# Kernel tuning notes

Measured on AMD Instinct MI355X. Metric: run time of the kernel, lower is better.

The kernel has to match this reference:

```python
import jax, jax.numpy as jnp
import numpy as np

MODEL_DIM = 2048
HEAD_DIM = 64
STATE_DIM = 128
EXPAND = 2
CHUNK = 64
INNER = EXPAND * MODEL_DIM          # 4096
NHEADS = INNER // HEAD_DIM          # 64
IN_PROJ = INNER + 2 * STATE_DIM + NHEADS  # 4416
B_SZ = 2
SEQ = 4096


def segsum(x):
    """Stable segment sum: x (..., T) -> (..., T, T) with -inf above diagonal."""
    T = x.shape[-1]
    mask_strict = jnp.tril(jnp.ones((T, T), dtype=bool), -1)
    # element [d, e] = x[d] on strictly-lower triangle, 0 elsewhere
    xt = jnp.where(mask_strict, x[..., :, None], 0.0)
    seg = jnp.cumsum(xt, axis=-2)
    mask = jnp.tril(jnp.ones((T, T), dtype=bool), 0)
    return jnp.where(mask, seg, -jnp.inf)


def ssd(x, A, B, C, chunk):
    """Mamba-2 SSD. x:(b,L,h,p), A:(b,L,h), B/C:(b,L,n) shared over heads."""
    b, L, h, p = x.shape
    n = B.shape[-1]
    c = L // chunk
    x = x.reshape(b, c, chunk, h, p)
    A = A.reshape(b, c, chunk, h).transpose(0, 3, 1, 2)  # (b,h,c,l)
    B = B.reshape(b, c, chunk, n)
    C = C.reshape(b, c, chunk, n)

    A_cs = jnp.cumsum(A, axis=-1)                        # (b,h,c,l)
    Lm = jnp.exp(segsum(A))                              # (b,h,c,l,l)
    # 1. diagonal (intra-chunk) output
    Y_diag = jnp.einsum('bcln,bcsn,bhcls,bcshp->bclhp', C, B, Lm, x)
    # 2. per-chunk states
    decay_states = jnp.exp(A_cs[..., -1:] - A_cs)        # (b,h,c,l)
    states = jnp.einsum('bcln,bhcl,bclhp->bchpn', B, decay_states, x)
    states = jnp.concatenate([jnp.zeros_like(states[:, :1]), states], axis=1)
    # 3. inter-chunk recurrence
    A_chunk = jnp.pad(A_cs[..., -1], ((0, 0), (0, 0), (1, 0)))   # (b,h,c+1)
    decay_chunk = jnp.exp(segsum(A_chunk))               # (b,h,c+1,c+1)
    new_states = jnp.einsum('bhzc,bchpn->bzhpn', decay_chunk, states)
    states_prev, final_state = new_states[:, :-1], new_states[:, -1]
    # 4. state -> output
    Y_off = jnp.einsum('bcln,bchpn,bhcl->bclhp', C, states_prev, jnp.exp(A_cs))
    Y = (Y_diag + Y_off).reshape(b, L, h, p)
    return Y, final_state


def setup_inputs() -> dict:
    key = jax.random.key(0)
    ks = jax.random.split(key, 6)
    u = jax.random.normal(ks[0], (B_SZ, SEQ, MODEL_DIM), jnp.float32)
    W_in = jax.random.normal(ks[1], (IN_PROJ, MODEL_DIM), jnp.float32) * 0.02
    b_in = jnp.zeros((IN_PROJ,), jnp.float32)
    W_out = jax.random.normal(ks[2], (MODEL_DIM, INNER), jnp.float32) * 0.02
    b_out = jnp.zeros((MODEL_DIM,), jnp.float32)
    # A_log = log(uniform(1, 16)) per Mamba-2 init
    A_log = jnp.log(jax.random.uniform(ks[3], (NHEADS,), jnp.float32, 1.0, 16.0))
    # dt_bias = inv-softplus of dt ~ loguniform(1e-3, 1e-1)
    dt = jnp.exp(jax.random.uniform(ks[4], (NHEADS,), jnp.float32)
                 * (np.log(0.1) - np.log(0.001)) + np.log(0.001))
    dt = jnp.clip(dt, 1e-4, None)
    dt_bias = dt + jnp.log(-jnp.expm1(-dt))
    return {'u': u, 'W_in': W_in, 'b_in': b_in, 'W_out': W_out,
            'b_out': b_out, 'A_log': A_log, 'dt_bias': dt_bias}


def reference(u, W_in, b_in, W_out, b_out, A_log, dt_bias):
    xBCdt = u @ W_in.T + b_in                       # (b, L, IN_PROJ)
    x, Bm, Cm, dt = jnp.split(
        xBCdt, [INNER, INNER + STATE_DIM, INNER + 2 * STATE_DIM], axis=-1)
    A = -jnp.exp(A_log)                             # (h,)
    dt = jax.nn.softplus(dt + dt_bias)              # (b, L, h)
    x = x.reshape(B_SZ, SEQ, NHEADS, HEAD_DIM)
    y, final_state = ssd(x * dt[..., None], A * dt, Bm, Cm, CHUNK)
    y = y.reshape(B_SZ, SEQ, INNER)
    y = y @ W_out.T + b_out
    return y, final_state
```

## Files before the change

kernel.cpp:

```cpp
#include <hip/hip_runtime.h>
#include <hip/hip_bf16.h>

typedef __hip_bfloat16 bf16;
typedef __attribute__((ext_vector_type(8))) short short8;
typedef __attribute__((ext_vector_type(4))) float f32x4;

#define MODEL_DIM 2048
#define INNER     4096
#define NHEADS    64
#define HEAD_DIM  64
#define STATE_DIM 128
#define IN_PROJ   4416
#define BSZ       2
#define SEQ       4096
#define CHUNKL    64
#define NTOK      (BSZ*SEQ)
#define NCHUNK    (SEQ/CHUNKL)

#define WAITV0() asm volatile("s_waitcnt vmcnt(0)" ::: "memory")
#define BAR()    __builtin_amdgcn_s_barrier()
#define SCHEDB() __builtin_amdgcn_sched_barrier(0)
#define WAITLG(N) do { asm volatile("s_waitcnt lgkmcnt(" #N ")" ::: "memory"); SCHEDB(); } while (0)

#define SWZ(x) ((x) ^ ((((x) >> 7) & 7) << 4))

static __device__ __forceinline__ void gload_lds16(const bf16* g, bf16* l) {
  __builtin_amdgcn_global_load_lds((const __attribute__((address_space(1))) void*)g,
                                   (__attribute__((address_space(3))) void*)l, 16, 0, 0);
}

static __device__ __forceinline__ unsigned lds_u32(const void* p) {
  return (unsigned)(unsigned long long)(const __attribute__((address_space(3))) char*)p;
}

static __device__ __forceinline__ short8 ds_read128(unsigned addr) {
  short8 r;
  asm volatile("ds_read_b128 %0, %1" : "=v"(r) : "v"(addr));
  return r;
}

static __device__ __forceinline__ void stage_unit(const bf16* __restrict__ P, int K,
                                                  int blockRow, int kt,
                                                  char* region, int unit, int t) {
  int o = unit * 8192 + (t << 4);
  int lb = SWZ(o);
  int row = lb >> 7, colb = lb & 127;
  gload_lds16(P + (size_t)(blockRow + row) * K + kt + (colb >> 1), (bf16*)(region + o));
}

#define MFMA_BLK(MLO, MHI, NLO, NHI)                                                    \
  __builtin_amdgcn_s_setprio(1);                                                       \
  _Pragma("unroll") for (int mf = (MLO); mf < (MHI); ++mf)                             \
    _Pragma("unroll") for (int nf = (NLO); nf < (NHI); ++nf)                           \
      _Pragma("unroll") for (int ks = 0; ks < 2; ++ks)                                 \
        acc[mf][nf] = __builtin_amdgcn_mfma_f32_16x16x32_bf16(a[mf][ks], b[nf][ks],    \
                                                              acc[mf][nf], 0, 0, 0);  \
  __builtin_amdgcn_s_setprio(0);

template<int BN>
static __device__ __forceinline__ void gemm_core1(
    const bf16* __restrict__ Ag, const bf16* __restrict__ Bg,
    int K, int NT, int bm, int bn, char* lds, f32x4 (&acc)[8][BN / 64]) {
  constexpr int NR = BN / 64;
  constexpr int BB = 32768 + NR * 8192;
  const int t = threadIdx.x;
  const int lane = t & 63;
  const int wid = t >> 6, wm = wid >> 2, wn = wid & 3;
  const unsigned x16 = (unsigned)(lane & 7) << 4;
  const unsigned kb0 = (unsigned)(lane >> 4) << 4;
  const unsigned ldsB = lds_u32(lds);
  const unsigned aRow0 = (unsigned)(wm * 128 + (lane & 15)) * 128;
  const unsigned bRow0 = (unsigned)(wn * (BN / 4) + (lane & 15)) * 128;

#pragma unroll
  for (int u = 0; u < 4; ++u) stage_unit(Ag, K, bm, 0, lds, u, t);
#pragma unroll
  for (int u = 0; u < NR; ++u) stage_unit(Bg, K, bn, 0, lds + 32768, u, t);
  WAITV0();
  BAR();

  int cur = 0;
  for (int tt = 0; tt < NT; ++tt) {
    char* oth = lds + (cur ^ 1) * BB;
    const unsigned aB = ldsB + (unsigned)(cur * BB);
    const unsigned bB = aB + 32768;
    const bool st = (tt + 1 < NT);

    if (st) {
      const int kt1 = (tt + 1) * 64;
#pragma unroll
      for (int u = 0; u < 4; ++u) stage_unit(Ag, K, bm, kt1, oth, u, t);
#pragma unroll
      for (int u = 0; u < NR; ++u) stage_unit(Bg, K, bn, kt1, oth + 32768, u, t);
    }

    short8 a[8][2], b[NR][2];
#pragma unroll
    for (int mf = 0; mf < 4; ++mf)
#pragma unroll
      for (int ks = 0; ks < 2; ++ks)
        a[mf][ks] = ds_read128(aB + aRow0 + mf * 2048 + (((unsigned)(ks * 64) + kb0) ^ x16));
#pragma unroll
    for (int nf = 0; nf < 2; ++nf)
#pragma unroll
      for (int ks = 0; ks < 2; ++ks)
        b[nf][ks] = ds_read128(bB + bRow0 + nf * 2048 + (((unsigned)(ks * 64) + kb0) ^ x16));
#pragma unroll
    for (int mf = 4; mf < 8; ++mf)
#pragma unroll
      for (int ks = 0; ks < 2; ++ks)
        a[mf][ks] = ds_read128(aB + aRow0 + mf * 2048 + (((unsigned)(ks * 64) + kb0) ^ x16));
#pragma unroll
    for (int nf = 2; nf < NR; ++nf)
#pragma unroll
      for (int ks = 0; ks < 2; ++ks)
        b[nf][ks] = ds_read128(bB + bRow0 + nf * 2048 + (((unsigned)(ks * 64) + kb0) ^ x16));

    if constexpr (NR == 4) WAITLG(12); else WAITLG(10);
    MFMA_BLK(0, 4, 0, 2);
    if constexpr (NR == 4) WAITLG(4);  else WAITLG(2);
    MFMA_BLK(4, 8, 0, 2);
    WAITLG(0);
    MFMA_BLK(0, 8, 2, NR);

    if (st) WAITV0();
    BAR();
    cur ^= 1;
  }
}

__global__ __launch_bounds__(512, 2)
void gemm_in256(const bf16* __restrict__ A, const bf16* __restrict__ Bw,
                const float* __restrict__ bias, bf16* __restrict__ x_bf,
                bf16* __restrict__ B_bf, bf16* __restrict__ C_bf, float* __restrict__ dtraw) {
  __shared__ char lds[2 * (32768 + 3 * 8192)];
  int nwg = gridDim.x, bid = blockIdx.x;
  int cpx = nwg >> 3;
  int sb = (bid & 7) * cpx + (bid >> 3);
  int bx = sb % (IN_PROJ / 192), by = sb / (IN_PROJ / 192);
  int bm = by * 256, bn = bx * 192;
  f32x4 acc[8][3] = {};
  gemm_core1<192>(A, Bw, MODEL_DIM, MODEL_DIM / 64, bm, bn, lds, acc);
  const int lane = threadIdx.x & 63, wid = threadIdx.x >> 6;
  const int wm = wid >> 2, wn = wid & 3;
#pragma unroll
  for (int mf = 0; mf < 8; ++mf)
#pragma unroll
    for (int nf = 0; nf < 3; ++nf)
#pragma unroll
      for (int r = 0; r < 4; ++r) {
        int row = bm + wm * 128 + mf * 16 + (lane >> 4) * 4 + r;
        int col = bn + wn * 48 + nf * 16 + (lane & 15);
        float v = acc[mf][nf][r] + bias[col];
        if (col < 4096)       x_bf[(size_t)row * 4096 + col]         = __float2bfloat16(v);
        else if (col < 4224)  B_bf[(size_t)row * 128 + (col - 4096)] = __float2bfloat16(v);
        else if (col < 4352)  C_bf[(size_t)row * 128 + (col - 4224)] = __float2bfloat16(v);
        else                  dtraw[(size_t)row * 64 + (col - 4352)] = v;
      }
}

__global__ __launch_bounds__(512, 2)
void gemm_out256(const bf16* __restrict__ A, const bf16* __restrict__ Bw,
                 const float* __restrict__ bias, float* __restrict__ C) {
  __shared__ char lds[2 * (32768 + 4 * 8192)];
  int nwg = gridDim.x, bid = blockIdx.x;
  int cpx = nwg >> 3;
  int sb = (bid & 7) * cpx + (bid >> 3);
  int bx = sb % (MODEL_DIM / 256), by = sb / (MODEL_DIM / 256);
  int bm = by * 256, bn = bx * 256;
  f32x4 acc[8][4] = {};
  gemm_core1<256>(A, Bw, INNER, INNER / 64, bm, bn, lds, acc);
  const int lane = threadIdx.x & 63, wid = threadIdx.x >> 6;
  const int wm = wid >> 2, wn = wid & 3;
#pragma unroll
  for (int mf = 0; mf < 8; ++mf)
#pragma unroll
    for (int nf = 0; nf < 4; ++nf)
#pragma unroll
      for (int r = 0; r < 4; ++r) {
        int row = bm + wm * 128 + mf * 16 + (lane >> 4) * 4 + r;
        int col = bn + wn * 64 + nf * 16 + (lane & 15);
        C[(size_t)row * MODEL_DIM + col] = acc[mf][nf][r] + bias[col];
      }
}

__global__ __launch_bounds__(256) void conv_f32_to_bf16(const float* __restrict__ src,
                                                        bf16* __restrict__ dst, int n4) {
  int i = blockIdx.x * 256 + threadIdx.x;
  if (i >= n4) return;
  float4 v = *(const float4*)(src + (size_t)i * 4);
  bf16* d = dst + (size_t)i * 4;
  d[0] = __float2bfloat16(v.x); d[1] = __float2bfloat16(v.y);
  d[2] = __float2bfloat16(v.z); d[3] = __float2bfloat16(v.w);
}

__global__ __launch_bounds__(256)
void prep_small(const float* __restrict__ dtraw, const float* __restrict__ A_log,
                const float* __restrict__ dt_bias, float* __restrict__ dts,
                float* __restrict__ a_dt) {
  int i = blockIdx.x * 256 + threadIdx.x;
  int h = i & 63;
  float z = dtraw[i] + dt_bias[h];
  float dt = (z > 20.f) ? z : log1pf(expf(z));
  dts[i] = dt;
  a_dt[i] = -expf(A_log[h]) * dt;
}

__global__ __launch_bounds__(256)
void g_pre_kernel(const bf16* __restrict__ B_bf, const bf16* __restrict__ C_bf,
                  float* __restrict__ G_g) {
  __shared__ bf16 Cs[64 * 128];
  __shared__ bf16 Bs[64 * 128];
  int blk = blockIdx.x;
  int t = threadIdx.x, lane = t & 63, wid = t >> 6;
  int tokBase = (blk >> 6) * SEQ + (blk & 63) * 64;

#pragma unroll
  for (int i = 0; i < 4; ++i) {
    int chunk = t + i * 256;
    int l = chunk >> 4, n0 = (chunk & 15) * 8;
    *(short8*)(Cs + l * 128 + n0) = *(const short8*)(C_bf + (size_t)(tokBase + l) * 128 + n0);
    *(short8*)(Bs + l * 128 + n0) = *(const short8*)(B_bf + (size_t)(tokBase + l) * 128 + n0);
  }
  __syncthreads();

  int lBase = (wid >> 1) * 32, sBase = (wid & 1) * 32;
  f32x4 g[2][2] = {};
#pragma unroll
  for (int ks = 0; ks < 4; ++ks) {
    short8 a[2], bb[2];
#pragma unroll
    for (int mi = 0; mi < 2; ++mi)
      a[mi] = *(const short8*)(Cs + (lBase + mi * 16 + (lane & 15)) * 128 + ks * 32 + (lane >> 4) * 8);
#pragma unroll
    for (int ni = 0; ni < 2; ++ni)
      bb[ni] = *(const short8*)(Bs + (sBase + ni * 16 + (lane & 15)) * 128 + ks * 32 + (lane >> 4) * 8);
#pragma unroll
    for (int mi = 0; mi < 2; ++mi)
#pragma unroll
      for (int ni = 0; ni < 2; ++ni)
        g[mi][ni] = __builtin_amdgcn_mfma_f32_16x16x32_bf16(a[mi], bb[ni], g[mi][ni], 0, 0, 0);
  }
  float* Gd = G_g + (size_t)blk * 4096;
#pragma unroll
  for (int mi = 0; mi < 2; ++mi)
#pragma unroll
    for (int ni = 0; ni < 2; ++ni)
#pragma unroll
      for (int r = 0; r < 4; ++r) {
        int row = lBase + mi * 16 + (lane >> 4) * 4 + r;
        int col = sBase + ni * 16 + (lane & 15);
        Gd[row * 64 + col] = g[mi][ni][r];
      }
}

#define LP 72
__global__ __launch_bounds__(256)
void ssd_fused_kernel(const bf16* __restrict__ x_bf, const bf16* __restrict__ B_bf,
                      const float* __restrict__ dts_g, const float* __restrict__ a_dt,
                      float* __restrict__ acs_g, bf16* __restrict__ states_g,
                      float* __restrict__ out_fs) {
  __shared__ bf16 xT[2][32 * LP];
  __shared__ bf16 BT[2][128 * LP];
  __shared__ float sc_s[64];
  __shared__ float dfac_s[1];
  int blk = blockIdx.x;
  int pg = blk & 1, h = (blk >> 1) & 63, b = blk >> 7;
  int t = threadIdx.x, lane = t & 63, w = t >> 6;
  int lx = t >> 2, sx = t & 3;
  int lB = t >> 2, sB = t & 3;

  f32x4 S4[4] = {};
  short8 rx, rB[4]; float ra = 0.f, rdt = 0.f;
  {
    int tb = b * SEQ;
    rx = *(const short8*)(x_bf + (size_t)(tb + lx) * 4096 + h * 64 + pg * 32 + sx * 8);
#pragma unroll
    for (int k = 0; k < 4; ++k)
      rB[k] = *(const short8*)(B_bf + (size_t)(tb + lB) * 128 + sB * 32 + k * 8);
    if (t < 64) { ra = a_dt[(size_t)(tb + t) * 64 + h]; rdt = dts_g[(size_t)(tb + t) * 64 + h]; }
  }

  for (int c = 0; c < 64; ++c) {
    int cn = (c < 63) ? c + 1 : 63;
    int tbn = b * SEQ + cn * 64;
    short8 rx2 = *(const short8*)(x_bf + (size_t)(tbn + lx) * 4096 + h * 64 + pg * 32 + sx * 8);
    short8 rB2[4];
#pragma unroll
    for (int k = 0; k < 4; ++k)
      rB2[k] = *(const short8*)(B_bf + (size_t)(tbn + lB) * 128 + sB * 32 + k * 8);
    float ra2 = 0.f, rdt2 = 0.f;
    if (t < 64) { ra2 = a_dt[(size_t)(tbn + t) * 64 + h]; rdt2 = dts_g[(size_t)(tbn + t) * 64 + h]; }

    if (t < 64) {
      float v = ra;
#pragma unroll
      for (int d = 1; d < 64; d <<= 1) { float o = __shfl_up(v, d); if (t >= d) v += o; }
      float a63 = __shfl(v, 63);
      if (pg == 0) acs_g[(((size_t)(b * 64 + c)) * 64 + h) * 64 + t] = v;
      sc_s[t] = rdt * expf(a63 - v);
      if (t == 0) dfac_s[0] = expf(a63);
    }
    __syncthreads();

    int bufc = c & 1;
    float dfac = dfac_s[0];
    {
      float s_l = sc_s[lx];
      const bf16* pv = (const bf16*)&rx;
#pragma unroll
      for (int j = 0; j < 8; ++j)
        xT[bufc][(sx * 8 + j) * LP + lx] = __float2bfloat16(__bfloat162float(pv[j]) * s_l);
#pragma unroll
      for (int k = 0; k < 4; ++k) {
        const bf16* pb = (const bf16*)&rB[k];
        int n0 = sB * 32 + k * 8;
#pragma unroll
        for (int j = 0; j < 8; ++j) BT[bufc][(n0 + j) * LP + lB] = pb[j];
      }
    }
    __syncthreads();

    int ps = (w >> 1) * 16, nb = (w & 1) * 64;
    f32x4 acc[4] = {};
    short8 af[2];
#pragma unroll
    for (int ks = 0; ks < 2; ++ks)
      af[ks] = *(const short8*)(&xT[bufc][(ps + (lane & 15)) * LP + ks * 32 + (lane >> 4) * 8]);
#pragma unroll
    for (int nf = 0; nf < 4; ++nf)
#pragma unroll
      for (int ks = 0; ks < 2; ++ks) {
        short8 bf_ = *(const short8*)(&BT[bufc][(nb + nf * 16 + (lane & 15)) * LP + ks * 32 + (lane >> 4) * 8]);
        acc[nf] = __builtin_amdgcn_mfma_f32_16x16x32_bf16(af[ks], bf_, acc[nf], 0, 0, 0);
      }
    size_t sbase = ((size_t)((b * 64 + c) * 64 + h)) * 8192;
#pragma unroll
    for (int nf = 0; nf < 4; ++nf)
#pragma unroll
      for (int r = 0; r < 4; ++r) {
        int p = pg * 32 + ps + (lane >> 4) * 4 + r;
        int n = nb + nf * 16 + (lane & 15);
        states_g[sbase + (size_t)p * 128 + n] = __float2bfloat16(S4[nf][r]);
        S4[nf][r] = dfac * S4[nf][r] + acc[nf][r];
      }

    rx = rx2; ra = ra2; rdt = rdt2;
#pragma unroll
    for (int k = 0; k < 4; ++k) rB[k] = rB2[k];
  }

  size_t ob = ((size_t)(b * 64 + h)) * 8192;
  int ps = (w >> 1) * 16, nb = (w & 1) * 64;
#pragma unroll
  for (int nf = 0; nf < 4; ++nf)
#pragma unroll
    for (int r = 0; r < 4; ++r) {
      int p = pg * 32 + ps + (lane >> 4) * 4 + r;
      int n = nb + nf * 16 + (lane & 15);
      out_fs[ob + (size_t)p * 128 + n] = S4[nf][r];
    }
}

__global__ __launch_bounds__(256)
void ssd_out_kernel(bf16* __restrict__ x_bf, const bf16* __restrict__ C_bf,
                    const float* __restrict__ dts, const float* __restrict__ acs_g,
                    const bf16* __restrict__ states_g, const float* __restrict__ G_g) {
  __shared__ bf16 Cs[64 * 128];
  __shared__ bf16 Ms[64 * 64];
  __shared__ bf16 xT[64 * 64];
  __shared__ bf16 Sp[64 * 128];
  __shared__ float acs_s[64];
  int blk = blockIdx.x;
  int h = blk & 63, c = (blk >> 6) & 63, b = blk >> 12;
  int t = threadIdx.x, lane = t & 63, wid = t >> 6;
  int tokBase = b * SEQ + c * 64;
  size_t sbase = ((size_t)((b * 64 + c) * 64 + h)) * 8192;

  int lBase = (wid >> 1) * 32, sBase = (wid & 1) * 32;
  const float* Gd = G_g + ((size_t)(b * 64 + c)) * 4096;
  float gv[2][2][4];
#pragma unroll
  for (int mi = 0; mi < 2; ++mi)
#pragma unroll
    for (int ni = 0; ni < 2; ++ni)
#pragma unroll
      for (int r = 0; r < 4; ++r)
        gv[mi][ni][r] = Gd[(lBase + mi * 16 + (lane >> 4) * 4 + r) * 64 +
                           sBase + ni * 16 + (lane & 15)];

  if (t < 64) acs_s[t] = acs_g[(((size_t)(b * 64 + c)) * 64 + h) * 64 + t];
#pragma unroll
  for (int i = 0; i < 4; ++i) {
    int chunk = t + i * 256;
    int l = chunk >> 4, n0 = (chunk & 15) * 8;
    *(short8*)(Cs + l * 128 + n0) = *(const short8*)(C_bf + (size_t)(tokBase + l) * 128 + n0);
  }
#pragma unroll
  for (int i = 0; i < 2; ++i) {
    int chunk = t + i * 256;
    int l = chunk >> 3, p0 = (chunk & 7) * 8;
    float dtv = dts[(size_t)(tokBase + l) * 64 + h];
    short8 vv = *(const short8*)(x_bf + (size_t)(tokBase + l) * 4096 + h * 64 + p0);
    const bf16* pv = (const bf16*)&vv;
#pragma unroll
    for (int j = 0; j < 8; ++j)
      xT[(p0 + j) * 64 + l] = __float2bfloat16(__bfloat162float(pv[j]) * dtv);
  }
#pragma unroll
  for (int i = 0; i < 4; ++i) {
    int chunk = t + i * 256;
    *(short8*)(Sp + chunk * 8) = *(const short8*)(states_g + sbase + chunk * 8);
  }
  __syncthreads();

#pragma unroll
  for (int mi = 0; mi < 2; ++mi)
#pragma unroll
    for (int ni = 0; ni < 2; ++ni)
#pragma unroll
      for (int r = 0; r < 4; ++r) {
        int row = lBase + mi * 16 + (lane >> 4) * 4 + r;
        int col = sBase + ni * 16 + (lane & 15);
        float lm = (row >= col) ? expf(acs_s[row] - acs_s[col]) : 0.f;
        Ms[row * 64 + col] = __float2bfloat16(gv[mi][ni][r] * lm);
      }
  __syncthreads();

  int pBase = (wid & 1) * 32;
  f32x4 yd[2][2] = {}, yo[2][2] = {};
#pragma unroll
  for (int ks = 0; ks < 2; ++ks) {
    short8 a[2], bb[2];
#pragma unroll
    for (int mi = 0; mi < 2; ++mi)
      a[mi] = *(const short8*)(Ms + (lBase + mi * 16 + (lane & 15)) * 64 + ks * 32 + (lane >> 4) * 8);
#pragma unroll
    for (int ni = 0; ni < 2; ++ni)
      bb[ni] = *(const short8*)(xT + (pBase + ni * 16 + (lane & 15)) * 64 + ks * 32 + (lane >> 4) * 8);
#pragma unroll
    for (int mi = 0; mi < 2; ++mi)
#pragma unroll
      for (int ni = 0; ni < 2; ++ni)
        yd[mi][ni] = __builtin_amdgcn_mfma_f32_16x16x32_bf16(a[mi], bb[ni], yd[mi][ni], 0, 0, 0);
  }
#pragma unroll
  for (int ks = 0; ks < 4; ++ks) {
    short8 a[2], bb[2];
#pragma unroll
    for (int mi = 0; mi < 2; ++mi)
      a[mi] = *(const short8*)(Cs + (lBase + mi * 16 + (lane & 15)) * 128 + ks * 32 + (lane >> 4) * 8);
#pragma unroll
    for (int ni = 0; ni < 2; ++ni)
      bb[ni] = *(const short8*)(Sp + (pBase + ni * 16 + (lane & 15)) * 128 + ks * 32 + (lane >> 4) * 8);
#pragma unroll
    for (int mi = 0; mi < 2; ++mi)
#pragma unroll
      for (int ni = 0; ni < 2; ++ni)
        yo[mi][ni] = __builtin_amdgcn_mfma_f32_16x16x32_bf16(a[mi], bb[ni], yo[mi][ni], 0, 0, 0);
  }
  __syncthreads();
#pragma unroll
  for (int mi = 0; mi < 2; ++mi)
#pragma unroll
    for (int ni = 0; ni < 2; ++ni)
#pragma unroll
      for (int r = 0; r < 4; ++r) {
        int lr = lBase + mi * 16 + (lane >> 4) * 4 + r;
        int p = pBase + ni * 16 + (lane & 15);
        float val = yd[mi][ni][r] + expf(acs_s[lr]) * yo[mi][ni][r];
        x_bf[(size_t)(tokBase + lr) * 4096 + h * 64 + p] = __float2bfloat16(val);
      }
}

extern "C" void kernel_launch(void* const* d_in, const int* in_sizes, int n_in,
                              void* d_out, int out_size, void* d_ws, size_t ws_size,
                              hipStream_t stream) {
  const float* u       = (const float*)d_in[0];
  const float* W_in    = (const float*)d_in[1];
  const float* b_in    = (const float*)d_in[2];
  const float* W_out   = (const float*)d_in[3];
  const float* b_out   = (const float*)d_in[4];
  const float* A_log   = (const float*)d_in[5];
  const float* dt_bias = (const float*)d_in[6];

  float* y_out  = (float*)d_out;
  float* fs_out = y_out + (size_t)NTOK * MODEL_DIM;

  char* ws = (char*)d_ws;
  size_t off = 0;
  auto alloc = [&](size_t bytes) { char* p = ws + off; off += (bytes + 255) & ~255ull; return p; };
  bf16*  wout_bf = (bf16*) alloc((size_t)MODEL_DIM * INNER * 2);
  bf16*  x_bf    = (bf16*) alloc((size_t)NTOK * INNER * 2);
  bf16*  B_bf    = (bf16*) alloc((size_t)NTOK * STATE_DIM * 2);
  bf16*  C_bf    = (bf16*) alloc((size_t)NTOK * STATE_DIM * 2);
  float* dtraw   = (float*)alloc((size_t)NTOK * NHEADS * 4);
  float* dts     = (float*)alloc((size_t)NTOK * NHEADS * 4);
  float* a_dt    = (float*)alloc((size_t)NTOK * NHEADS * 4);
  float* acs     = (float*)alloc((size_t)BSZ * NCHUNK * NHEADS * 64 * 4);
  float* gbuf    = (float*)alloc((size_t)BSZ * NCHUNK * 4096 * 4);
  char*  Q       = alloc((size_t)BSZ * NCHUNK * NHEADS * 64 * 128 * 2);
  bf16*  states  = (bf16*)Q;
  bf16*  u_bf    = (bf16*)Q;
  bf16*  win_bf  = u_bf + (size_t)NTOK * MODEL_DIM;
  (void)ws_size; (void)off; (void)in_sizes; (void)n_in; (void)out_size;

  conv_f32_to_bf16<<<dim3(16384), dim3(256), 0, stream>>>(u, u_bf, NTOK * MODEL_DIM / 4);
  conv_f32_to_bf16<<<dim3(IN_PROJ * MODEL_DIM / 1024), dim3(256), 0, stream>>>(
      W_in, win_bf, IN_PROJ * MODEL_DIM / 4);
  conv_f32_to_bf16<<<dim3(8192), dim3(256), 0, stream>>>(W_out, wout_bf, MODEL_DIM * INNER / 4);

  gemm_in256<<<dim3((NTOK / 256) * (IN_PROJ / 192)), dim3(512), 0, stream>>>(
      u_bf, win_bf, b_in, x_bf, B_bf, C_bf, dtraw);

  prep_small<<<dim3(NTOK * NHEADS / 256), dim3(256), 0, stream>>>(dtraw, A_log, dt_bias, dts, a_dt);

  g_pre_kernel<<<dim3(BSZ * NCHUNK), dim3(256), 0, stream>>>(B_bf, C_bf, gbuf);

  ssd_fused_kernel<<<dim3(BSZ * NHEADS * 2), dim3(256), 0, stream>>>(
      x_bf, B_bf, dts, a_dt, acs, states, fs_out);

  ssd_out_kernel<<<dim3(BSZ * NCHUNK * NHEADS), dim3(256), 0, stream>>>(
      x_bf, C_bf, dts, acs, states, gbuf);

  gemm_out256<<<dim3((MODEL_DIM / 256) * (NTOK / 256)), dim3(512), 0, stream>>>(
      x_bf, wout_bf, b_out, y_out);
}
```

Baseline: 509.4 us.

## Deepen prefetch in SSD state scan and reuse C/G tiles across heads

The sequential chunk-state kernel now prefetches two chunks ahead and computes the next chunk's cumulative-sum scale factors before the barrier, removing one __syncthreads per iteration so global-load latency and the scan overlap with the MFMA work. The output kernel now processes four heads per block, loading the C tile and the G matrix once and reusing them across those heads, with a quarter as many blocks. The cost is more live registers in the scan kernel and less parallelism plus serialized per-head work in the output kernel.

After: 487.7 us, median of 3. -4.2%, faster.

```diff
diff --git a/kernel.cpp b/kernel.cpp
--- a/kernel.cpp
+++ b/kernel.cpp
@@ -262,65 +262,88 @@
                       float* __restrict__ out_fs) {
   __shared__ bf16 xT[2][32 * LP];
   __shared__ bf16 BT[2][128 * LP];
-  __shared__ float sc_s[64];
-  __shared__ float dfac_s[1];
+  __shared__ float sc_s[2][64];
+  __shared__ float dfac_s[4];
   int blk = blockIdx.x;
   int pg = blk & 1, h = (blk >> 1) & 63, b = blk >> 7;
   int t = threadIdx.x, lane = t & 63, w = t >> 6;
   int lx = t >> 2, sx = t & 3;
-  int lB = t >> 2, sB = t & 3;
 
   f32x4 S4[4] = {};
-  short8 rx, rB[4]; float ra = 0.f, rdt = 0.f;
+  short8 rxC, rBC[4], rxN, rBN[4];
+  float raN = 0.f, rdtN = 0.f;
+
   {
     int tb = b * SEQ;
-    rx = *(const short8*)(x_bf + (size_t)(tb + lx) * 4096 + h * 64 + pg * 32 + sx * 8);
+    rxC = *(const short8*)(x_bf + (size_t)(tb + lx) * 4096 + h * 64 + pg * 32 + sx * 8);
 #pragma unroll
     for (int k = 0; k < 4; ++k)
-      rB[k] = *(const short8*)(B_bf + (size_t)(tb + lB) * 128 + sB * 32 + k * 8);
-    if (t < 64) { ra = a_dt[(size_t)(tb + t) * 64 + h]; rdt = dts_g[(size_t)(tb + t) * 64 + h]; }
-  }
-
-  for (int c = 0; c < 64; ++c) {
-    int cn = (c < 63) ? c + 1 : 63;
-    int tbn = b * SEQ + cn * 64;
-    short8 rx2 = *(const short8*)(x_bf + (size_t)(tbn + lx) * 4096 + h * 64 + pg * 32 + sx * 8);
-    short8 rB2[4];
-#pragma unroll
-    for (int k = 0; k < 4; ++k)
-      rB2[k] = *(const short8*)(B_bf + (size_t)(tbn + lB) * 128 + sB * 32 + k * 8);
-    float ra2 = 0.f, rdt2 = 0.f;
-    if (t < 64) { ra2 = a_dt[(size_t)(tbn + t) * 64 + h]; rdt2 = dts_g[(size_t)(tbn + t) * 64 + h]; }
-
+      rBC[k] = *(const short8*)(B_bf + (size_t)(tb + lx) * 128 + sx * 32 + k * 8);
     if (t < 64) {
-      float v = ra;
+      float ra0 = a_dt[(size_t)(tb + t) * 64 + h];
+      float rdt0 = dts_g[(size_t)(tb + t) * 64 + h];
+      float v = ra0;
 #pragma unroll
       for (int d = 1; d < 64; d <<= 1) { float o = __shfl_up(v, d); if (t >= d) v += o; }
       float a63 = __shfl(v, 63);
-      if (pg == 0) acs_g[(((size_t)(b * 64 + c)) * 64 + h) * 64 + t] = v;
-      sc_s[t] = rdt * expf(a63 - v);
+      if (pg == 0) acs_g[(((size_t)(b * 64 + 0)) * 64 + h) * 64 + t] = v;
+      sc_s[0][t] = rdt0 * expf(a63 - v);
       if (t == 0) dfac_s[0] = expf(a63);
     }
-    __syncthreads();
+    int tb1 = tb + 64;
+    rxN = *(const short8*)(x_bf + (size_t)(tb1 + lx) * 4096 + h * 64 + pg * 32 + sx * 8);
+#pragma unroll
+    for (int k = 0; k < 4; ++k)
+      rBN[k] = *(const short8*)(B_bf + (size_t)(tb1 + lx) * 128 + sx * 32 + k * 8);
+    if (t < 64) {
+      raN = a_dt[(size_t)(tb1 + t) * 64 + h];
+      rdtN = dts_g[(size_t)(tb1 + t) * 64 + h];
+    }
+  }
+  __syncthreads();
+
+  for (int c = 0; c < 64; ++c) {
+    int c2 = (c < 62) ? c + 2 : 63;
+    int tb2 = b * SEQ + c2 * 64;
+    short8 rxI = *(const short8*)(x_bf + (size_t)(tb2 + lx) * 4096 + h * 64 + pg * 32 + sx * 8);
+    short8 rBI[4];
+#pragma unroll
+    for (int k = 0; k < 4; ++k)
+      rBI[k] = *(const short8*)(B_bf + (size_t)(tb2 + lx) * 128 + sx * 32 + k * 8);
+    float raI = 0.f, rdtI = 0.f;
+    if (t < 64) {
+      raI = a_dt[(size_t)(tb2 + t) * 64 + h];
+      rdtI = dts_g[(size_t)(tb2 + t) * 64 + h];
+    }
 
     int bufc = c & 1;
-    float dfac = dfac_s[0];
     {
-      float s_l = sc_s[lx];
-      const bf16* pv = (const bf16*)&rx;
+      float s_l = sc_s[bufc][lx];
+      const bf16* pv = (const bf16*)&rxC;
 #pragma unroll
       for (int j = 0; j < 8; ++j)
         xT[bufc][(sx * 8 + j) * LP + lx] = __float2bfloat16(__bfloat162float(pv[j]) * s_l);
 #pragma unroll
       for (int k = 0; k < 4; ++k) {
-        const bf16* pb = (const bf16*)&rB[k];
-        int n0 = sB * 32 + k * 8;
-#pragma unroll
-        for (int j = 0; j < 8; ++j) BT[bufc][(n0 + j) * LP + lB] = pb[j];
+        const bf16* pb = (const bf16*)&rBC[k];
+        int n0 = sx * 32 + k * 8;
+#pragma unroll
+        for (int j = 0; j < 8; ++j) BT[bufc][(n0 + j) * LP + lx] = pb[j];
       }
     }
+    if (t < 64) {
+      float v = raN;
+#pragma unroll
+      for (int d = 1; d < 64; d <<= 1) { float o = __shfl_up(v, d); if (t >= d) v += o; }
+      float a63 = __shfl(v, 63);
+      if (c + 1 < 64 && pg == 0)
+        acs_g[(((size_t)(b * 64 + c + 1)) * 64 + h) * 64 + t] = v;
+      sc_s[(c + 1) & 1][t] = rdtN * expf(a63 - v);
+      if (t == 0) dfac_s[(c + 1) & 3] = expf(a63);
+    }
     __syncthreads();
 
+    float dfac = dfac_s[c & 3];
     int ps = (w >> 1) * 16, nb = (w & 1) * 64;
     f32x4 acc[4] = {};
     short8 af[2];
@@ -345,9 +368,10 @@
         S4[nf][r] = dfac * S4[nf][r] + acc[nf][r];
       }
 
-    rx = rx2; ra = ra2; rdt = rdt2;
-#pragma unroll
-    for (int k = 0; k < 4; ++k) rB[k] = rB2[k];
+    rxC = rxN; rxN = rxI;
+#pragma unroll
+    for (int k = 0; k < 4; ++k) { rBC[k] = rBN[k]; rBN[k] = rBI[k]; }
+    raN = raI; rdtN = rdtI;
   }
 
   size_t ob = ((size_t)(b * 64 + h)) * 8192;
@@ -370,12 +394,11 @@
   __shared__ bf16 Ms[64 * 64];
   __shared__ bf16 xT[64 * 64];
   __shared__ bf16 Sp[64 * 128];
-  __shared__ float acs_s[64];
+  __shared__ float acs_s[2][64];
   int blk = blockIdx.x;
-  int h = blk & 63, c = (blk >> 6) & 63, b = blk >> 12;
+  int hg = blk & 15, c = (blk >> 4) & 63, b = blk >> 10;
   int t = threadIdx.x, lane = t & 63, wid = t >> 6;
   int tokBase = b * SEQ + c * 64;
-  size_t sbase = ((size_t)((b * 64 + c) * 64 + h)) * 8192;
 
   int lBase = (wid >> 1) * 32, sBase = (wid & 1) * 32;
   const float* Gd = G_g + ((size_t)(b * 64 + c)) * 4096;
@@ -389,88 +412,95 @@
         gv[mi][ni][r] = Gd[(lBase + mi * 16 + (lane >> 4) * 4 + r) * 64 +
                            sBase + ni * 16 + (lane & 15)];
 
-  if (t < 64) acs_s[t] = acs_g[(((size_t)(b * 64 + c)) * 64 + h) * 64 + t];
 #pragma unroll
   for (int i = 0; i < 4; ++i) {
     int chunk = t + i * 256;
     int l = chunk >> 4, n0 = (chunk & 15) * 8;
     *(short8*)(Cs + l * 128 + n0) = *(const short8*)(C_bf + (size_t)(tokBase + l) * 128 + n0);
   }
-#pragma unroll
-  for (int i = 0; i < 2; ++i) {
-    int chunk = t + i * 256;
-    int l = chunk >> 3, p0 = (chunk & 7) * 8;
-    float dtv = dts[(size_t)(tokBase + l) * 64 + h];
-    short8 vv = *(const short8*)(x_bf + (size_t)(tokBase + l) * 4096 + h * 64 + p0);
-    const bf16* pv = (const bf16*)&vv;
-#pragma unroll
-    for (int j = 0; j < 8; ++j)
-      xT[(p0 + j) * 64 + l] = __float2bfloat16(__bfloat162float(pv[j]) * dtv);
-  }
-#pragma unroll
-  for (int i = 0; i < 4; ++i) {
-    int chunk = t + i * 256;
-    *(short8*)(Sp + chunk * 8) = *(const short8*)(states_g + sbase + chunk * 8);
-  }
-  __syncthreads();
-
-#pragma unroll
-  for (int mi = 0; mi < 2; ++mi)
-#pragma unroll
-    for (int ni = 0; ni < 2; ++ni)
-#pragma unroll
-      for (int r = 0; r < 4; ++r) {
-        int row = lBase + mi * 16 + (lane >> 4) * 4 + r;
-        int col = sBase + ni * 16 + (lane & 15);
-        float lm = (row >= col) ? expf(acs_s[row] - acs_s[col]) : 0.f;
-        Ms[row * 64 + col] = __float2bfloat16(gv[mi][ni][r] * lm);
-      }
-  __syncthreads();
-
-  int pBase = (wid & 1) * 32;
-  f32x4 yd[2][2] = {}, yo[2][2] = {};
-#pragma unroll
-  for (int ks = 0; ks < 2; ++ks) {
-    short8 a[2], bb[2];
+
+  for (int hi = 0; hi < 4; ++hi) {
+    int h = hg * 4 + hi;
+    size_t sbase = ((size_t)((b * 64 + c) * 64 + h)) * 8192;
+
+    if (t < 64) acs_s[hi & 1][t] = acs_g[(((size_t)(b * 64 + c)) * 64 + h) * 64 + t];
+#pragma unroll
+    for (int i = 0; i < 2; ++i) {
+      int chunk = t + i * 256;
+      int l = chunk >> 3, p0 = (chunk & 7) * 8;
+      float dtv = dts[(size_t)(tokBase + l) * 64 + h];
+      short8 vv = *(const short8*)(x_bf + (size_t)(tokBase + l) * 4096 + h * 64 + p0);
+      const bf16* pv = (const bf16*)&vv;
+#pragma unroll
+      for (int j = 0; j < 8; ++j)
+        xT[(p0 + j) * 64 + l] = __float2bfloat16(__bfloat162float(pv[j]) * dtv);
+    }
+#pragma unroll
+    for (int i = 0; i < 4; ++i) {
+      int chunk = t + i * 256;
+      *(short8*)(Sp + chunk * 8) = *(const short8*)(states_g + sbase + chunk * 8);
+    }
+    __syncthreads();
+
 #pragma unroll
     for (int mi = 0; mi < 2; ++mi)
-      a[mi] = *(const short8*)(Ms + (lBase + mi * 16 + (lane & 15)) * 64 + ks * 32 + (lane >> 4) * 8);
-#pragma unroll
-    for (int ni = 0; ni < 2; ++ni)
-      bb[ni] = *(const short8*)(xT + (pBase + ni * 16 + (lane & 15)) * 64 + ks * 32 + (lane >> 4) * 8);
+#pragma unroll
+      for (int ni = 0; ni < 2; ++ni)
+#pragma unroll
+        for (int r = 0; r < 4; ++r) {
+          int row = lBase + mi * 16 + (lane >> 4) * 4 + r;
+          int col = sBase + ni * 16 + (lane & 15);
+          float lm = (row >= col) ? expf(acs_s[hi & 1][row] - acs_s[hi & 1][col]) : 0.f;
+          Ms[row * 64 + col] = __float2bfloat16(gv[mi][ni][r] * lm);
+        }
+    __syncthreads();
+
+    int pBase = (wid & 1) * 32;
+    f32x4 yd[2][2] = {}, yo[2][2] = {};
+#pragma unroll
+    for (int ks = 0; ks < 2; ++ks) {
+      short8 a[2], bb[2];
+#pragma unroll
+      for (int mi = 0; mi < 2; ++mi)
+        a[mi] = *(const short8*)(Ms + (lBase + mi * 16 + (lane & 15)) * 64 + ks * 32 + (lane >> 4) * 8);
+#pragma unroll
+      for (int ni = 0; ni < 2; ++ni)
+        bb[ni] = *(const short8*)(xT + (pBase + ni * 16 + (lane & 15)) * 64 + ks * 32 + (lane >> 4) * 8);
+#pragma unroll
+      for (int mi = 0; mi < 2; ++mi)
+#pragma unroll
+        for (int ni = 0; ni < 2; ++ni)
+          yd[mi][ni] = __builtin_amdgcn_mfma_f32_16x16x32_bf16(a[mi], bb[ni], yd[mi][ni], 0, 0, 0);
+    }
+#pragma unroll
+    for (int ks = 0; ks < 4; ++ks) {
+      short8 a[2], bb[2];
+#pragma unroll
+      for (int mi = 0; mi < 2; ++mi)
+        a[mi] = *(const short8*)(Cs + (lBase + mi * 16 + (lane & 15)) * 128 + ks * 32 + (lane >> 4) * 8);
+#pragma unroll
+      for (int ni = 0; ni < 2; ++ni)
+        bb[ni] = *(const short8*)(Sp + (pBase + ni * 16 + (lane & 15)) * 128 + ks * 32 + (lane >> 4) * 8);
+#pragma unroll
+      for (int mi = 0; mi < 2; ++mi)
+#pragma unroll
+        for (int ni = 0; ni < 2; ++ni)
+          yo[mi][ni] = __builtin_amdgcn_mfma_f32_16x16x32_bf16(a[mi], bb[ni], yo[mi][ni], 0, 0, 0);
+    }
+    __syncthreads();
+
 #pragma unroll
     for (int mi = 0; mi < 2; ++mi)
 #pragma unroll
       for (int ni = 0; ni < 2; ++ni)
-        yd[mi][ni] = __builtin_amdgcn_mfma_f32_16x16x32_bf16(a[mi], bb[ni], yd[mi][ni], 0, 0, 0);
-  }
-#pragma unroll
-  for (int ks = 0; ks < 4; ++ks) {
-    short8 a[2], bb[2];
-#pragma unroll
-    for (int mi = 0; mi < 2; ++mi)
-      a[mi] = *(const short8*)(Cs + (lBase + mi * 16 + (lane & 15)) * 128 + ks * 32 + (lane >> 4) * 8);
-#pragma unroll
-    for (int ni = 0; ni < 2; ++ni)
-      bb[ni] = *(const short8*)(Sp + (pBase + ni * 16 + (lane & 15)) * 128 + ks * 32 + (lane >> 4) * 8);
-#pragma unroll
-    for (int mi = 0; mi < 2; ++mi)
-#pragma unroll
-      for (int ni = 0; ni < 2; ++ni)
-        yo[mi][ni] = __builtin_amdgcn_mfma_f32_16x16x32_bf16(a[mi], bb[ni], yo[mi][ni], 0, 0, 0);
-  }
-  __syncthreads();
-#pragma unroll
-  for (int mi = 0; mi < 2; ++mi)
-#pragma unroll
-    for (int ni = 0; ni < 2; ++ni)
-#pragma unroll
-      for (int r = 0; r < 4; ++r) {
-        int lr = lBase + mi * 16 + (lane >> 4) * 4 + r;
-        int p = pBase + ni * 16 + (lane & 15);
-        float val = yd[mi][ni][r] + expf(acs_s[lr]) * yo[mi][ni][r];
-        x_bf[(size_t)(tokBase + lr) * 4096 + h * 64 + p] = __float2bfloat16(val);
-      }
+#pragma unroll
+        for (int r = 0; r < 4; ++r) {
+          int lr = lBase + mi * 16 + (lane >> 4) * 4 + r;
+          int p = pBase + ni * 16 + (lane & 15);
+          float val = yd[mi][ni][r] + expf(acs_s[hi & 1][lr]) * yo[mi][ni][r];
+          x_bf[(size_t)(tokBase + lr) * 4096 + h * 64 + p] = __float2bfloat16(val);
+        }
+  }
 }
 
 extern "C" void kernel_launch(void* const* d_in, const int* in_sizes, int n_in,
@@ -520,7 +550,7 @@
   ssd_fused_kernel<<<dim3(BSZ * NHEADS * 2), dim3(256), 0, stream>>>(
       x_bf, B_bf, dts, a_dt, acs, states, fs_out);
 
-  ssd_out_kernel<<<dim3(BSZ * NCHUNK * NHEADS), dim3(256), 0, stream>>>(
+  ssd_out_kernel<<<dim3(BSZ * NCHUNK * 16), dim3(256), 0, stream>>>(
       x_bf, C_bf, dts, acs, states, gbuf);
 
   gemm_out256<<<dim3((MODEL_DIM / 256) * (NTOK / 256)), dim3(512), 0, stream>>>(
```
